# Kernel tuning notes

Hardware: AMD Instinct MI355X
Metric: run time of the kernel (lower is better)

Reference implementation:

```python
import jax, jax.numpy as jnp
import numpy as np

N = 1048576          # query points
L = 16               # hash levels per encoding
T = 524288           # 2**19 hashmap entries per level
F = 2                # features per level
BASE = 16.0
GROWTH = 1.3819      # per_level_scale so level 15 ~ 2048
RES = np.asarray(BASE * GROWTH ** np.arange(L), dtype=np.float32)
PRIME0 = np.uint32(1)
PRIME1 = np.uint32(2654435761)


def hashgrid_encode(points, table):
    """points: [N,2] in [0,1); table: [L,T,F] -> [N, L*F]."""
    def level(tab, res):
        pos = points * res                      # [N,2]
        pf = jnp.floor(pos)
        w = pos - pf                            # bilinear weights [N,2]
        pi = pf.astype(jnp.int32)

        def corner(dx, dy):
            c = (pi + jnp.array([dx, dy], jnp.int32)).astype(jnp.uint32)
            h = (c[:, 0] * PRIME0) ^ (c[:, 1] * PRIME1)
            return tab[(h % jnp.uint32(T)).astype(jnp.int32)]  # [N,F]

        wx, wy = w[:, 0:1], w[:, 1:2]
        return (corner(0, 0) * (1 - wx) * (1 - wy)
                + corner(1, 0) * wx * (1 - wy)
                + corner(0, 1) * (1 - wx) * wy
                + corner(1, 1) * wx * wy)       # [N,F]

    feats = jax.vmap(level)(table, jnp.asarray(RES))   # [L,N,F]
    return jnp.transpose(feats, (1, 0, 2)).reshape(points.shape[0], L * F)


def setup_inputs() -> dict:
    key = jax.random.key(0)
    ks = jax.random.split(key, 10)
    pts = {name: jax.random.uniform(ks[i], (N, 2), dtype=jnp.float32)
           for i, name in enumerate(
               ['points_xy', 'points_xz', 'points_yz', 'points_xt', 'points_yt', 'points_zt'])}
    tables = (jax.random.uniform(ks[6], (6, L, T, F), dtype=jnp.float32) * 2e-4 - 1e-4)
    d_in = 6 * L * F + 6 * 2   # 204
    W1 = jax.random.normal(ks[7], (d_in, 64), dtype=jnp.float32) / np.float32(np.sqrt(d_in))
    W2 = jax.random.normal(ks[8], (64, 64), dtype=jnp.float32) / np.float32(8.0)
    W3 = jax.random.normal(ks[9], (64, 3), dtype=jnp.float32) / np.float32(8.0)
    return {**pts, 'tables': tables, 'W1': W1, 'W2': W2, 'W3': W3}


def reference(points_xy, points_xz, points_yz, points_xt, points_yt, points_zt,
              tables, W1, W2, W3):
    pts = [points_xy, points_xz, points_yz, points_xt, points_yt, points_zt]
    parts = []
    for i in range(6):                       # fixed structural loop over 6 planes
        parts.append(hashgrid_encode(pts[i], tables[i]))
        parts.append(pts[i])
    enc = jnp.concatenate(parts, axis=-1)    # [N, 204]
    h = jax.nn.relu(enc @ W1)
    h = jax.nn.relu(h @ W2)
    return h @ W3                            # [N, 3]
```

## Files before the change

### kernel.cpp

```cpp
#include <hip/hip_runtime.h>

#define THREADS 256
#define LVLS 16
#define TSZ 524288u
#define TMASK 524287u
#define PRIME1 2654435761u
#define HID 64
#define NBIN 4096
#define ENC_STRIDE 104
#define MLP_TILES 8

typedef __attribute__((ext_vector_type(8))) short bf16x8;
typedef __attribute__((ext_vector_type(4))) float f32x4;

constexpr float resf(int l) { double r = 16.0; for (int i = 0; i < l; ++i) r *= 1.3819; return (float)r; }

__device__ __constant__ float c_RES[LVLS] = {
    resf(0),  resf(1),  resf(2),  resf(3),
    resf(4),  resf(5),  resf(6),  resf(7),
    resf(8),  resf(9),  resf(10), resf(11),
    resf(12), resf(13), resf(14), resf(15)
};

__device__ __forceinline__ unsigned packbf2(float a, float b) {
    unsigned ua = __float_as_uint(a), ub = __float_as_uint(b);
    ua += 0x7FFFu + ((ua >> 16) & 1u);
    ub += 0x7FFFu + ((ub >> 16) & 1u);
    return (ua >> 16) | (ub & 0xFFFF0000u);
}

__device__ __forceinline__ unsigned short bf16rne(float f) {
    unsigned u = __float_as_uint(f);
    u += 0x7FFFu + ((u >> 16) & 1u);
    return (unsigned short)(u >> 16);
}

__device__ __forceinline__ unsigned part1by1(unsigned v) {
    v &= 0xFFu;
    v = (v | (v << 4)) & 0x0F0Fu;
    v = (v | (v << 2)) & 0x3333u;
    v = (v | (v << 1)) & 0x5555u;
    return v;
}

__device__ __forceinline__ float2 load_pt(int s, int i,
    const float* pxy, const float* pxz, const float* pyz,
    const float* pxt, const float* pyt, const float* pzt)
{
    switch (s) {
        case 0: return ((const float2*)pxy)[i];
        case 1: return ((const float2*)pxz)[i];
        case 2: return ((const float2*)pyz)[i];
        case 3: return ((const float2*)pxt)[i];
        case 4: return ((const float2*)pyt)[i];
        default: return ((const float2*)pzt)[i];
    }
}

__device__ __forceinline__ unsigned bin_key(float2 pt) {
    const int xb = min(63, (int)(pt.x * 64.f));
    const int yb = min(63, (int)(pt.y * 64.f));
    return part1by1((unsigned)xb) | (part1by1((unsigned)yb) << 1);
}

__global__ __launch_bounds__(256) void pack_w1_k(const float* __restrict__ W1,
                                                 unsigned short* __restrict__ W1B)
{
    const int e = blockIdx.x * 256 + threadIdx.x;
    if (e >= 7 * 4 * 64 * 8) return;
    const int j = e & 7;
    const int lane = (e >> 3) & 63;
    const int n = (e >> 9) & 3;
    const int t = e >> 11;
    const int k = t * 32 + ((lane >> 4) << 3) + j;
    const int col = n * 16 + (lane & 15);
    float v = 0.f;
    if (k < 192) { const int s = k >> 5, rem = k & 31; v = W1[(s * 34 + rem) * HID + col]; }
    else if (k < 204) { const int q = k - 192; v = W1[((q >> 1) * 34 + 32 + (q & 1)) * HID + col]; }
    W1B[e] = bf16rne(v);
}

__global__ __launch_bounds__(256) void pack_w2_k(const float* __restrict__ W2,
                                                 unsigned short* __restrict__ W2B)
{
    const int e = blockIdx.x * 256 + threadIdx.x;
    if (e >= 2 * 4 * 64 * 8) return;
    const int j = e & 7;
    const int lane = (e >> 3) & 63;
    const int n = (e >> 9) & 3;
    const int t = e >> 11;
    const int k = t * 32 + ((lane >> 4) << 3) + j;
    const int col = n * 16 + (lane & 15);
    W2B[e] = bf16rne(W2[k * HID + col]);
}

__global__ void zero_hist_k(int* __restrict__ hist) {
    const int i = blockIdx.x * blockDim.x + threadIdx.x;
    if (i < 6 * NBIN) hist[i] = 0;
}

__global__ __launch_bounds__(THREADS) void hist_k(
    const float* __restrict__ pxy, const float* __restrict__ pxz,
    const float* __restrict__ pyz, const float* __restrict__ pxt,
    const float* __restrict__ pyt, const float* __restrict__ pzt,
    int* __restrict__ hist, int npts, int bpp)
{
    const int s = blockIdx.x / bpp;
    const int i = (blockIdx.x - s * bpp) * THREADS + threadIdx.x;
    if (i >= npts) return;
    const float2 pt = load_pt(s, i, pxy, pxz, pyz, pxt, pyt, pzt);
    atomicAdd(&hist[s * NBIN + bin_key(pt)], 1);
}

__global__ __launch_bounds__(1024) void scan_k(
    const int* __restrict__ hist, int* __restrict__ curs)
{
    __shared__ int sb[1024];
    const int p = blockIdx.x;
    const int t = threadIdx.x;
    const int h0 = hist[p * NBIN + 4 * t + 0];
    const int h1 = hist[p * NBIN + 4 * t + 1];
    const int h2 = hist[p * NBIN + 4 * t + 2];
    const int h3 = hist[p * NBIN + 4 * t + 3];
    const int i1 = h0 + h1;
    const int i2 = i1 + h2;
    const int i3 = i2 + h3;
    sb[t] = i3;
    __syncthreads();
    for (int off = 1; off < 1024; off <<= 1) {
        const int v = (t >= off) ? sb[t - off] : 0;
        __syncthreads();
        sb[t] += v;
        __syncthreads();
    }
    const int start = sb[t] - i3;
    curs[p * NBIN + 4 * t + 0] = start;
    curs[p * NBIN + 4 * t + 1] = start + h0;
    curs[p * NBIN + 4 * t + 2] = start + i1;
    curs[p * NBIN + 4 * t + 3] = start + i2;
}

__global__ __launch_bounds__(THREADS) void scatter_k(
    const float* __restrict__ pxy, const float* __restrict__ pxz,
    const float* __restrict__ pyz, const float* __restrict__ pxt,
    const float* __restrict__ pyt, const float* __restrict__ pzt,
    int* __restrict__ curs, int* __restrict__ sidx, int npts, int bpp)
{
    const int s = blockIdx.x / bpp;
    const int i = (blockIdx.x - s * bpp) * THREADS + threadIdx.x;
    if (i >= npts) return;
    const float2 pt = load_pt(s, i, pxy, pxz, pyz, pxt, pyt, pzt);
    const int pos = atomicAdd(&curs[s * NBIN + bin_key(pt)], 1);
    sidx[(size_t)s * npts + pos] = i;
}

__global__ __launch_bounds__(THREADS, 6) void gather_sorted_k(
    const float* __restrict__ pxy, const float* __restrict__ pxz,
    const float* __restrict__ pyz, const float* __restrict__ pxt,
    const float* __restrict__ pyt, const float* __restrict__ pzt,
    const float* __restrict__ tables, const int* __restrict__ sidx,
    unsigned* __restrict__ encW, int npts, int bpp)
{
    const int s = blockIdx.x / bpp;
    const int i = (blockIdx.x - s * bpp) * THREADS + threadIdx.x;
    if (i >= npts) return;

    const int orig = sidx[(size_t)s * npts + i];
    const float2 pt = load_pt(s, orig, pxy, pxz, pyz, pxt, pyt, pzt);
    const float2* tbase = ((const float2*)tables) + (size_t)s * LVLS * TSZ;

    unsigned ew[LVLS];
    #pragma unroll
    for (int l = 0; l < LVLS; ++l) {
        const float r = c_RES[l];
        const float fx = pt.x * r, fy = pt.y * r;
        const float flx = floorf(fx), fly = floorf(fy);
        const float wx = fx - flx, wy = fy - fly;
        const unsigned x0 = (unsigned)(int)flx;
        const unsigned y0 = (unsigned)(int)fly;
        const unsigned hy0 = y0 * PRIME1;
        const unsigned hy1 = hy0 + PRIME1;
        const float2* tab = tbase + (size_t)l * TSZ;
        const float2 f00 = tab[(x0 ^ hy0) & TMASK];
        const float2 f10 = tab[((x0 + 1u) ^ hy0) & TMASK];
        const float2 f01 = tab[(x0 ^ hy1) & TMASK];
        const float2 f11 = tab[((x0 + 1u) ^ hy1) & TMASK];
        const float w00 = (1.f - wx) * (1.f - wy);
        const float w10 = wx * (1.f - wy);
        const float w01 = (1.f - wx) * wy;
        const float w11 = wx * wy;
        const float e0 = f00.x * w00 + f10.x * w10 + f01.x * w01 + f11.x * w11;
        const float e1 = f00.y * w00 + f10.y * w10 + f01.y * w01 + f11.y * w11;
        ew[l] = packbf2(e0, e1);
    }

    unsigned* rowp = encW + (size_t)orig * ENC_STRIDE;
    uint4* dst = (uint4*)(rowp + s * LVLS);
    dst[0] = make_uint4(ew[0],  ew[1],  ew[2],  ew[3]);
    dst[1] = make_uint4(ew[4],  ew[5],  ew[6],  ew[7]);
    dst[2] = make_uint4(ew[8],  ew[9],  ew[10], ew[11]);
    dst[3] = make_uint4(ew[12], ew[13], ew[14], ew[15]);
    rowp[96 + s] = packbf2(pt.x, pt.y);
    if (s == 0) { rowp[102] = 0u; rowp[103] = 0u; }
}

__global__ __launch_bounds__(256, 2) void mlp_mfma_k(
    const unsigned* __restrict__ encW, const unsigned short* __restrict__ W1Bg,
    const unsigned short* __restrict__ W2Bg, const float* __restrict__ W3,
    float* __restrict__ out, int npts)
{
    __shared__ uint4 sW1B[1792];
    __shared__ uint4 sW2B[512];
    __shared__ float sW3[192];
    __shared__ unsigned short sH1[4][1024];

    const int tid = threadIdx.x;
    for (int i = tid; i < 1792; i += 256) sW1B[i] = ((const uint4*)W1Bg)[i];
    for (int i = tid; i < 512; i += 256) sW2B[i] = ((const uint4*)W2Bg)[i];
    for (int i = tid; i < 192; i += 256) sW3[i] = W3[i];
    __syncthreads();

    const int w = tid >> 6, lane = tid & 63;
    const int row = lane & 15, g = lane >> 4;
    const int blk0 = blockIdx.x * (64 * MLP_TILES);

    for (int it = 0; it < MLP_TILES; ++it) {
        const int p0 = blk0 + (it * 4 + w) * 16;
        if (p0 + 16 > npts) { __syncthreads(); __syncthreads(); continue; }

        f32x4 acc0 = {0.f,0.f,0.f,0.f}, acc1 = acc0, acc2_ = acc0, acc3 = acc0;
        const unsigned* arow = encW + (size_t)(p0 + row) * ENC_STRIDE;
        #pragma unroll
        for (int t = 0; t < 7; ++t) {
            const int gw = (t == 6) ? (g & 1) : g;
            const uint4 av = *(const uint4*)(arow + t * 16 + gw * 4);
            const bf16x8 a = *(const bf16x8*)&av;
            acc0 = __builtin_amdgcn_mfma_f32_16x16x32_bf16(a, *(const bf16x8*)&sW1B[(t*4+0)*64 + lane], acc0, 0, 0, 0);
            acc1 = __builtin_amdgcn_mfma_f32_16x16x32_bf16(a, *(const bf16x8*)&sW1B[(t*4+1)*64 + lane], acc1, 0, 0, 0);
            acc2_ = __builtin_amdgcn_mfma_f32_16x16x32_bf16(a, *(const bf16x8*)&sW1B[(t*4+2)*64 + lane], acc2_, 0, 0, 0);
            acc3 = __builtin_amdgcn_mfma_f32_16x16x32_bf16(a, *(const bf16x8*)&sW1B[(t*4+3)*64 + lane], acc3, 0, 0, 0);
        }

        #pragma unroll
        for (int r = 0; r < 4; ++r) {
            const int rr = g * 4 + r;
            const int base = rr * 64;
            const int swz = (rr & 7) << 3;
            sH1[w][(base + 0 * 16 + row) ^ swz] = bf16rne(fmaxf(acc0[r], 0.f));
            sH1[w][(base + 1 * 16 + row) ^ swz] = bf16rne(fmaxf(acc1[r], 0.f));
            sH1[w][(base + 2 * 16 + row) ^ swz] = bf16rne(fmaxf(acc2_[r], 0.f));
            sH1[w][(base + 3 * 16 + row) ^ swz] = bf16rne(fmaxf(acc3[r], 0.f));
        }
        __syncthreads();

        f32x4 b0 = {0.f,0.f,0.f,0.f}, b1 = b0, b2 = b0, b3 = b0;
        #pragma unroll
        for (int t = 0; t < 2; ++t) {
            const int kidx = (row * 64 + t * 32 + g * 8) ^ ((row & 7) << 3);
            const bf16x8 a2 = *(const bf16x8*)&sH1[w][kidx];
            b0 = __builtin_amdgcn_mfma_f32_16x16x32_bf16(a2, *(const bf16x8*)&sW2B[(t*4+0)*64 + lane], b0, 0, 0, 0);
            b1 = __builtin_amdgcn_mfma_f32_16x16x32_bf16(a2, *(const bf16x8*)&sW2B[(t*4+1)*64 + lane], b1, 0, 0, 0);
            b2 = __builtin_amdgcn_mfma_f32_16x16x32_bf16(a2, *(const bf16x8*)&sW2B[(t*4+2)*64 + lane], b2, 0, 0, 0);
            b3 = __builtin_amdgcn_mfma_f32_16x16x32_bf16(a2, *(const bf16x8*)&sW2B[(t*4+3)*64 + lane], b3, 0, 0, 0);
        }

        float o[4][3];
        #pragma unroll
        for (int r = 0; r < 4; ++r) { o[r][0] = 0.f; o[r][1] = 0.f; o[r][2] = 0.f; }
        #pragma unroll
        for (int n = 0; n < 4; ++n) {
            const int m = n * 16 + row;
            const float w30 = sW3[m * 3 + 0], w31 = sW3[m * 3 + 1], w32 = sW3[m * 3 + 2];
            const f32x4 bb = (n == 0) ? b0 : (n == 1) ? b1 : (n == 2) ? b2 : b3;
            #pragma unroll
            for (int r = 0; r < 4; ++r) {
                const float h = fmaxf(bb[r], 0.f);
                o[r][0] += h * w30; o[r][1] += h * w31; o[r][2] += h * w32;
            }
        }
        #pragma unroll
        for (int m = 1; m < 16; m <<= 1) {
            #pragma unroll
            for (int r = 0; r < 4; ++r) {
                o[r][0] += __shfl_xor(o[r][0], m, 64);
                o[r][1] += __shfl_xor(o[r][1], m, 64);
                o[r][2] += __shfl_xor(o[r][2], m, 64);
            }
        }
        if (row == 0) {
            #pragma unroll
            for (int r = 0; r < 4; ++r) {
                const int p = p0 + g * 4 + r;
                out[p * 3 + 0] = o[r][0];
                out[p * 3 + 1] = o[r][1];
                out[p * 3 + 2] = o[r][2];
            }
        }
        __syncthreads();
    }
}

__global__ __launch_bounds__(THREADS, 4) void fused_mono(
    const float* __restrict__ pxy, const float* __restrict__ pxz,
    const float* __restrict__ pyz, const float* __restrict__ pxt,
    const float* __restrict__ pyt, const float* __restrict__ pzt,
    const float* __restrict__ tables, const float* __restrict__ W1,
    const float* __restrict__ W2, const float* __restrict__ W3,
    float* __restrict__ out, int npts)
{
    const int gid = blockIdx.x * THREADS + threadIdx.x;

    float h1[HID];
    #pragma unroll
    for (int k = 0; k < HID; ++k) h1[k] = 0.f;

    #pragma unroll 1
    for (int s = 0; s < 6; ++s) {
        const float2 pt = load_pt(s, gid, pxy, pxz, pyz, pxt, pyt, pzt);
        const float px = pt.x, py = pt.y;
        const float2* tbase = ((const float2*)tables) + (size_t)s * LVLS * TSZ;
        const float* w1s = W1 + (s * 34) * HID;

        #pragma unroll 2
        for (int l = 0; l < LVLS; ++l) {
            const float r = c_RES[l];
            const float fx = px * r, fy = py * r;
            const float flx = floorf(fx), fly = floorf(fy);
            const float wx = fx - flx, wy = fy - fly;
            const unsigned x0 = (unsigned)(int)flx;
            const unsigned y0 = (unsigned)(int)fly;
            const unsigned hy0 = y0 * PRIME1;
            const unsigned hy1 = hy0 + PRIME1;
            const float2* tab = tbase + (size_t)l * TSZ;
            const float2 f00 = tab[(x0 ^ hy0) & TMASK];
            const float2 f10 = tab[((x0 + 1u) ^ hy0) & TMASK];
            const float2 f01 = tab[(x0 ^ hy1) & TMASK];
            const float2 f11 = tab[((x0 + 1u) ^ hy1) & TMASK];
            const float w00 = (1.f - wx) * (1.f - wy);
            const float w10 = wx * (1.f - wy);
            const float w01 = (1.f - wx) * wy;
            const float w11 = wx * wy;
            const float e0 = f00.x * w00 + f10.x * w10 + f01.x * w01 + f11.x * w11;
            const float e1 = f00.y * w00 + f10.y * w10 + f01.y * w01 + f11.y * w11;
            const float4* wa = (const float4*)(w1s + (2 * l) * HID);
            const float4* wb = wa + 16;
            #pragma unroll
            for (int q = 0; q < 16; ++q) {
                const float4 a = wa[q];
                const float4 b = wb[q];
                h1[4*q+0] += e0 * a.x + e1 * b.x;
                h1[4*q+1] += e0 * a.y + e1 * b.y;
                h1[4*q+2] += e0 * a.z + e1 * b.z;
                h1[4*q+3] += e0 * a.w + e1 * b.w;
            }
        }
        const float4* wa = (const float4*)(w1s + 32 * HID);
        const float4* wb = wa + 16;
        #pragma unroll
        for (int q = 0; q < 16; ++q) {
            const float4 a = wa[q];
            const float4 b = wb[q];
            h1[4*q+0] += px * a.x + py * b.x;
            h1[4*q+1] += px * a.y + py * b.y;
            h1[4*q+2] += px * a.z + py * b.z;
            h1[4*q+3] += px * a.w + py * b.w;
        }
    }

    #pragma unroll
    for (int k = 0; k < HID; ++k) h1[k] = fmaxf(h1[k], 0.f);

    float o0 = 0.f, o1 = 0.f, o2 = 0.f;
    #pragma unroll 1
    for (int c = 0; c < 4; ++c) {
        float t[16];
        #pragma unroll
        for (int i = 0; i < 16; ++i) t[i] = 0.f;
        #pragma unroll
        for (int k = 0; k < HID; ++k) {
            const float4* w2r = (const float4*)(W2 + k * HID + c * 16);
            const float hk = h1[k];
            const float4 a = w2r[0];
            const float4 b = w2r[1];
            const float4 d = w2r[2];
            const float4 e = w2r[3];
            t[0]  += hk * a.x;  t[1]  += hk * a.y;  t[2]  += hk * a.z;  t[3]  += hk * a.w;
            t[4]  += hk * b.x;  t[5]  += hk * b.y;  t[6]  += hk * b.z;  t[7]  += hk * b.w;
            t[8]  += hk * d.x;  t[9]  += hk * d.y;  t[10] += hk * d.z;  t[11] += hk * d.w;
            t[12] += hk * e.x;  t[13] += hk * e.y;  t[14] += hk * e.z;  t[15] += hk * e.w;
        }
        #pragma unroll
        for (int i = 0; i < 16; ++i) {
            const float tt = fmaxf(t[i], 0.f);
            const int m = c * 16 + i;
            o0 += tt * W3[m * 3 + 0];
            o1 += tt * W3[m * 3 + 1];
            o2 += tt * W3[m * 3 + 2];
        }
    }

    if (gid < npts) {
        out[3 * gid + 0] = o0;
        out[3 * gid + 1] = o1;
        out[3 * gid + 2] = o2;
    }
}

extern "C" void kernel_launch(void* const* d_in, const int* in_sizes, int n_in,
                              void* d_out, int out_size, void* d_ws, size_t ws_size,
                              hipStream_t stream)
{
    const float* pxy = (const float*)d_in[0];
    const float* pxz = (const float*)d_in[1];
    const float* pyz = (const float*)d_in[2];
    const float* pxt = (const float*)d_in[3];
    const float* pyt = (const float*)d_in[4];
    const float* pzt = (const float*)d_in[5];
    const float* tables = (const float*)d_in[6];
    const float* W1 = (const float*)d_in[7];
    const float* W2 = (const float*)d_in[8];
    const float* W3 = (const float*)d_in[9];
    float* out = (float*)d_out;

    const int npts = in_sizes[0] / 2;
    const int bpp = (npts + THREADS - 1) / THREADS;

    const size_t off_hist = 0;
    const size_t off_curs = off_hist + (size_t)6 * NBIN * 4;
    const size_t off_w1b  = off_curs + (size_t)6 * NBIN * 4;
    const size_t off_w2b  = off_w1b + 28672;
    const size_t off_sidx = 256 * 1024;
    size_t off_enc = off_sidx + (size_t)6 * npts * 4;
    off_enc = (off_enc + 127) & ~(size_t)127;
    const size_t need = off_enc + (size_t)npts * ENC_STRIDE * 4;

    if (ws_size >= need && (npts % (64 * MLP_TILES)) == 0) {
        char* ws = (char*)d_ws;
        int* hist = (int*)(ws + off_hist);
        int* curs = (int*)(ws + off_curs);
        unsigned short* W1B = (unsigned short*)(ws + off_w1b);
        unsigned short* W2B = (unsigned short*)(ws + off_w2b);
        int* sidx = (int*)(ws + off_sidx);
        unsigned* encW = (unsigned*)(ws + off_enc);

        hipLaunchKernelGGL(zero_hist_k, dim3((6 * NBIN + THREADS - 1) / THREADS),
                           dim3(THREADS), 0, stream, hist);
        hipLaunchKernelGGL(hist_k, dim3(6 * bpp), dim3(THREADS), 0, stream,
                           pxy, pxz, pyz, pxt, pyt, pzt, hist, npts, bpp);
        hipLaunchKernelGGL(scan_k, dim3(6), dim3(1024), 0, stream, hist, curs);
        hipLaunchKernelGGL(pack_w1_k, dim3(56), dim3(256), 0, stream, W1, W1B);
        hipLaunchKernelGGL(pack_w2_k, dim3(16), dim3(256), 0, stream, W2, W2B);
        hipLaunchKernelGGL(scatter_k, dim3(6 * bpp), dim3(THREADS), 0, stream,
                           pxy, pxz, pyz, pxt, pyt, pzt, curs, sidx, npts, bpp);
        hipLaunchKernelGGL(gather_sorted_k, dim3(6 * bpp), dim3(THREADS), 0, stream,
                           pxy, pxz, pyz, pxt, pyt, pzt, tables, sidx, encW, npts, bpp);
        hipLaunchKernelGGL(mlp_mfma_k, dim3(npts / (64 * MLP_TILES)), dim3(256), 0, stream,
                           encW, W1B, W2B, W3, out, npts);
    } else {
        hipLaunchKernelGGL(fused_mono, dim3(bpp), dim3(THREADS), 0, stream,
                           pxy, pxz, pyz, pxt, pyt, pzt, tables, W1, W2, W3, out, npts);
    }
}
```

Measured before the change: 1.482 ms.

## Refine spatial binning, cache sort keys, and swizzle gather blocks across XCDs

Raises the Morton bin grid from 64x64 to 128x128 so sorted points are spatially tighter and table gathers get more cache locality. Each point's bin key is stored as a ushort in the histogram pass, so the scatter pass no longer reloads points or recomputes keys. The scan now runs in place and writes cursors back over the histogram, and the keys and histogram live in the encoding buffer before it is written. The gather kernel remaps block ids so consecutive blocks of the same plane land on the same XCD, which aims to improve L2 reuse of table entries. The costs are a larger scan and more histogram atomics over more bins, plus reliance on the assumption that there are 8 XCDs.

After: 1.471 ms. Within noise of the previous version (-0.7%).

```diff
diff --git a/kernel.cpp b/kernel.cpp
--- a/kernel.cpp
+++ b/kernel.cpp
@@ -6,7 +6,7 @@
 #define TMASK 524287u
 #define PRIME1 2654435761u
 #define HID 64
-#define NBIN 4096
+#define NBIN 16384
 #define ENC_STRIDE 104
 #define MLP_TILES 8
 
@@ -58,8 +58,8 @@
 }
 
 __device__ __forceinline__ unsigned bin_key(float2 pt) {
-    const int xb = min(63, (int)(pt.x * 64.f));
-    const int yb = min(63, (int)(pt.y * 64.f));
+    const int xb = min(127, (int)(pt.x * 128.f));
+    const int yb = min(127, (int)(pt.y * 128.f));
     return part1by1((unsigned)xb) | (part1by1((unsigned)yb) << 1);
 }
 
@@ -103,29 +103,28 @@
     const float* __restrict__ pxy, const float* __restrict__ pxz,
     const float* __restrict__ pyz, const float* __restrict__ pxt,
     const float* __restrict__ pyt, const float* __restrict__ pzt,
-    int* __restrict__ hist, int npts, int bpp)
+    int* __restrict__ hist, unsigned short* __restrict__ keys, int npts, int bpp)
 {
     const int s = blockIdx.x / bpp;
     const int i = (blockIdx.x - s * bpp) * THREADS + threadIdx.x;
     if (i >= npts) return;
     const float2 pt = load_pt(s, i, pxy, pxz, pyz, pxt, pyt, pzt);
-    atomicAdd(&hist[s * NBIN + bin_key(pt)], 1);
-}
-
-__global__ __launch_bounds__(1024) void scan_k(
-    const int* __restrict__ hist, int* __restrict__ curs)
+    const unsigned key = bin_key(pt);
+    keys[(size_t)s * npts + i] = (unsigned short)key;
+    atomicAdd(&hist[s * NBIN + key], 1);
+}
+
+__global__ __launch_bounds__(1024) void scan_k(int* __restrict__ hist)
 {
     __shared__ int sb[1024];
     const int p = blockIdx.x;
     const int t = threadIdx.x;
-    const int h0 = hist[p * NBIN + 4 * t + 0];
-    const int h1 = hist[p * NBIN + 4 * t + 1];
-    const int h2 = hist[p * NBIN + 4 * t + 2];
-    const int h3 = hist[p * NBIN + 4 * t + 3];
-    const int i1 = h0 + h1;
-    const int i2 = i1 + h2;
-    const int i3 = i2 + h3;
-    sb[t] = i3;
+    const int base = p * NBIN + t * 16;
+    int h[16], pre[16];
+    int run = 0;
+    #pragma unroll
+    for (int i = 0; i < 16; ++i) { h[i] = hist[base + i]; pre[i] = run; run += h[i]; }
+    sb[t] = run;
     __syncthreads();
     for (int off = 1; off < 1024; off <<= 1) {
         const int v = (t >= off) ? sb[t - off] : 0;
@@ -133,24 +132,20 @@
         sb[t] += v;
         __syncthreads();
     }
-    const int start = sb[t] - i3;
-    curs[p * NBIN + 4 * t + 0] = start;
-    curs[p * NBIN + 4 * t + 1] = start + h0;
-    curs[p * NBIN + 4 * t + 2] = start + i1;
-    curs[p * NBIN + 4 * t + 3] = start + i2;
+    const int start = sb[t] - run;
+    #pragma unroll
+    for (int i = 0; i < 16; ++i) hist[base + i] = start + pre[i];
 }
 
 __global__ __launch_bounds__(THREADS) void scatter_k(
-    const float* __restrict__ pxy, const float* __restrict__ pxz,
-    const float* __restrict__ pyz, const float* __restrict__ pxt,
-    const float* __restrict__ pyt, const float* __restrict__ pzt,
-    int* __restrict__ curs, int* __restrict__ sidx, int npts, int bpp)
+    const unsigned short* __restrict__ keys, int* __restrict__ curs,
+    int* __restrict__ sidx, int npts, int bpp)
 {
     const int s = blockIdx.x / bpp;
     const int i = (blockIdx.x - s * bpp) * THREADS + threadIdx.x;
     if (i >= npts) return;
-    const float2 pt = load_pt(s, i, pxy, pxz, pyz, pxt, pyt, pzt);
-    const int pos = atomicAdd(&curs[s * NBIN + bin_key(pt)], 1);
+    const unsigned key = keys[(size_t)s * npts + i];
+    const int pos = atomicAdd(&curs[s * NBIN + key], 1);
     sidx[(size_t)s * npts + pos] = i;
 }
 
@@ -161,8 +156,14 @@
     const float* __restrict__ tables, const int* __restrict__ sidx,
     unsigned* __restrict__ encW, int npts, int bpp)
 {
-    const int s = blockIdx.x / bpp;
-    const int i = (blockIdx.x - s * bpp) * THREADS + threadIdx.x;
+    int bid = blockIdx.x;
+    const int G = gridDim.x;
+    if ((G & 7) == 0) {
+        const int chunk = G >> 3;
+        bid = (bid & 7) * chunk + (bid >> 3);
+    }
+    const int s = bid / bpp;
+    const int i = (bid - s * bpp) * THREADS + threadIdx.x;
     if (i >= npts) return;
 
     const int orig = sidx[(size_t)s * npts + i];
@@ -425,33 +426,31 @@
     const int npts = in_sizes[0] / 2;
     const int bpp = (npts + THREADS - 1) / THREADS;
 
-    const size_t off_hist = 0;
-    const size_t off_curs = off_hist + (size_t)6 * NBIN * 4;
-    const size_t off_w1b  = off_curs + (size_t)6 * NBIN * 4;
-    const size_t off_w2b  = off_w1b + 28672;
-    const size_t off_sidx = 256 * 1024;
+    const size_t off_w1b  = 0;
+    const size_t off_w2b  = 28672;
+    const size_t off_sidx = 65536;
     size_t off_enc = off_sidx + (size_t)6 * npts * 4;
     off_enc = (off_enc + 127) & ~(size_t)127;
     const size_t need = off_enc + (size_t)npts * ENC_STRIDE * 4;
 
-    if (ws_size >= need && (npts % (64 * MLP_TILES)) == 0) {
+    if (ws_size >= need && (npts % (64 * MLP_TILES)) == 0 && npts % THREADS == 0) {
         char* ws = (char*)d_ws;
-        int* hist = (int*)(ws + off_hist);
-        int* curs = (int*)(ws + off_curs);
         unsigned short* W1B = (unsigned short*)(ws + off_w1b);
         unsigned short* W2B = (unsigned short*)(ws + off_w2b);
         int* sidx = (int*)(ws + off_sidx);
         unsigned* encW = (unsigned*)(ws + off_enc);
+        unsigned short* keys = (unsigned short*)encW;
+        int* hist = (int*)((char*)encW + (size_t)6 * npts * 2);
 
         hipLaunchKernelGGL(zero_hist_k, dim3((6 * NBIN + THREADS - 1) / THREADS),
                            dim3(THREADS), 0, stream, hist);
         hipLaunchKernelGGL(hist_k, dim3(6 * bpp), dim3(THREADS), 0, stream,
-                           pxy, pxz, pyz, pxt, pyt, pzt, hist, npts, bpp);
-        hipLaunchKernelGGL(scan_k, dim3(6), dim3(1024), 0, stream, hist, curs);
+                           pxy, pxz, pyz, pxt, pyt, pzt, hist, keys, npts, bpp);
+        hipLaunchKernelGGL(scan_k, dim3(6), dim3(1024), 0, stream, hist);
         hipLaunchKernelGGL(pack_w1_k, dim3(56), dim3(256), 0, stream, W1, W1B);
         hipLaunchKernelGGL(pack_w2_k, dim3(16), dim3(256), 0, stream, W2, W2B);
         hipLaunchKernelGGL(scatter_k, dim3(6 * bpp), dim3(THREADS), 0, stream,
-                           pxy, pxz, pyz, pxt, pyt, pzt, curs, sidx, npts, bpp);
+                           keys, hist, sidx, npts, bpp);
         hipLaunchKernelGGL(gather_sorted_k, dim3(6 * bpp), dim3(THREADS), 0, stream,
                            pxy, pxz, pyz, pxt, pyt, pzt, tables, sidx, encW, npts, bpp);
         hipLaunchKernelGGL(mlp_mfma_k, dim3(npts / (64 * MLP_TILES)), dim3(256), 0, stream,
```
